# Kernel optimization log

Measured on AMD Instinct MI355X. Metric: run time of the kernel, lower is better.

The kernel has to match this reference:

```python
import jax, jax.numpy as jnp
import numpy as np
import math

B, S, N, D, H = 4, 64, 256, 512, 8
DEPTH = D // H

def setup_inputs() -> dict:
    key = jax.random.key(0)
    ks = jax.random.split(key, 9)
    scale = 1.0 / math.sqrt(D)
    return {
        "x": jax.random.normal(ks[0], (B, S, N, D), dtype=jnp.float32),
        "Wq": jax.random.normal(ks[1], (D, D), dtype=jnp.float32) * scale,
        "bq": jax.random.normal(ks[2], (D,), dtype=jnp.float32) * 0.01,
        "Wk": jax.random.normal(ks[3], (D, D), dtype=jnp.float32) * scale,
        "bk": jax.random.normal(ks[4], (D,), dtype=jnp.float32) * 0.01,
        "Wv": jax.random.normal(ks[5], (D, D), dtype=jnp.float32) * scale,
        "bv": jax.random.normal(ks[6], (D,), dtype=jnp.float32) * 0.01,
        "Wo": jax.random.normal(ks[7], (D, D), dtype=jnp.float32) * scale,
        "bo": jax.random.normal(ks[8], (D,), dtype=jnp.float32) * 0.01,
    }

def _split_heads(t):
    # (B, S, M, D) -> (B, H, S, M, depth); matches split_head.forward (4D path)
    # followed by the att_dim==2 permute(0, 2, 1, 3, 4) in cross_attention.
    b, s, m, _ = t.shape
    return t.reshape(b, s, m, H, DEPTH).transpose(0, 3, 1, 2, 4)

def reference(x, Wq, bq, Wk, bk, Wv, bv, Wo, bo):
    b, s, n, d = x.shape
    # att_dim == 2: query is the cls token along the joint/patch axis.
    q = _split_heads(x[:, :, 0:1, :] @ Wq + bq)   # (B, H, S, 1, depth)
    k = _split_heads(x @ Wk + bk)                  # (B, H, S, N, depth)
    v = _split_heads(x @ Wv + bv)                  # (B, H, S, N, depth)
    # scaled dot product attention (mask is None in cross_attention)
    logits = jnp.einsum('bhsqd,bhskd->bhsqk', q, k) / math.sqrt(DEPTH)
    attn = jax.nn.softmax(logits, axis=-1)         # (B, H, S, 1, N)
    ctx = jnp.einsum('bhsqk,bhskd->bhsqd', attn, v)  # (B, H, S, 1, depth)
    # permute(0, 2, 3, 1, 4) then reshape (B, S, 1, D)
    concat = ctx.transpose(0, 2, 3, 1, 4).reshape(b, s, 1, d)
    return concat @ Wo + bo
```

## Files before the change

### kernel.cpp

```cpp
#include <hip/hip_runtime.h>
#include <stdint.h>
#include <math.h>


#define NT 32

__global__ __launch_bounds__(512) void fused_kernel(
    const float* __restrict__ x,
    const float* __restrict__ Wq, const float* __restrict__ bq,
    const float* __restrict__ Wk,
    const float* __restrict__ Wv, const float* __restrict__ bv,
    const float* __restrict__ Wo, const float* __restrict__ bo,
    float* __restrict__ out) {
  const int bs = blockIdx.x;
  const int t = threadIdx.x;
  const int w = t >> 6, lane = t & 63;
  const float* xb = x + (long)bs * 131072;

  __shared__ float x_tile[NT * 512];
  __shared__ float r_s[4096];
  __shared__ float y_s[8 * 520];
  __shared__ float q_s[512];
  __shared__ float x0_s[512];
  __shared__ float ctx_s[512];
  __shared__ float red_s[3][512];
  __shared__ float pt_s[8][NT];
  __shared__ float f_s[8], s_s[8];

  if (t < 128) *(float4*)&x0_s[t * 4] = *(const float4*)&xb[t * 4];
  __syncthreads();

  {
    const int j4 = (t & 127) * 4;
    const int kq = t >> 7;
    float4 a = make_float4(0.f, 0.f, 0.f, 0.f);
    const float* wp = Wq + (long)(kq * 128) * 512 + j4;
    const float* ap = &x0_s[kq * 128];
#pragma unroll 8
    for (int k = 0; k < 128; ++k) {
      float4 wv = *(const float4*)&wp[(long)k * 512];
      float av = ap[k];
      a.x += av * wv.x; a.y += av * wv.y; a.z += av * wv.z; a.w += av * wv.w;
    }
    if (kq > 0) *(float4*)&red_s[kq - 1][j4] = a;
    __syncthreads();
    if (kq == 0) {
#pragma unroll
      for (int rr = 0; rr < 3; ++rr) {
        float4 b = *(const float4*)&red_s[rr][j4];
        a.x += b.x; a.y += b.y; a.z += b.z; a.w += b.w;
      }
      float4 bb = *(const float4*)&bq[j4];
      a.x += bb.x; a.y += bb.y; a.z += bb.z; a.w += bb.w;
      *(float4*)&q_s[j4] = a;
    }
  }
  __syncthreads();

  {
    const float* wrow = Wk + (long)t * 512;
    for (int h = 0; h < 8; ++h) {
      float racc = 0.f;
      const float* qp = &q_s[h * 64];
#pragma unroll
      for (int c4 = 0; c4 < 16; ++c4) {
        float4 wv = *(const float4*)&wrow[h * 64 + c4 * 4];
        racc += qp[c4 * 4 + 0] * wv.x + qp[c4 * 4 + 1] * wv.y +
                qp[c4 * 4 + 2] * wv.z + qp[c4 * 4 + 3] * wv.w;
      }
      r_s[h * 512 + t] = racc;
    }
  }
  __syncthreads();

  float rv[8][8];
#pragma unroll
  for (int h = 0; h < 8; ++h) {
    float4 a = *(const float4*)&r_s[h * 512 + lane * 8];
    float4 b = *(const float4*)&r_s[h * 512 + lane * 8 + 4];
    rv[h][0] = a.x; rv[h][1] = a.y; rv[h][2] = a.z; rv[h][3] = a.w;
    rv[h][4] = b.x; rv[h][5] = b.y; rv[h][6] = b.z; rv[h][7] = b.w;
  }

  float accy[8] = {0.f, 0.f, 0.f, 0.f, 0.f, 0.f, 0.f, 0.f};
  float m_h = -INFINITY, s_h = 0.f;
  const int l4 = lane & 4, l2 = lane & 2, l1 = lane & 1;

  for (int tile = 0; tile < 8; ++tile) {
    {
      const float* src = xb + (long)tile * NT * 512;
#pragma unroll
      for (int i = 0; i < 8; ++i) {
        int f4 = t + i * 512;
        *(float4*)&x_tile[f4 * 4] = *(const float4*)&src[f4 * 4];
      }
    }
    __syncthreads();

#pragma unroll
    for (int i = 0; i < 4; ++i) {
      const int nl = w * 4 + i;
      const float* xr = &x_tile[nl * 512 + lane * 8];
      float4 xa = *(const float4*)xr;
      float4 xb4 = *(const float4*)(xr + 4);
      float acc[8];
#pragma unroll
      for (int h = 0; h < 8; ++h)
        acc[h] = xa.x * rv[h][0] + xa.y * rv[h][1] + xa.z * rv[h][2] + xa.w * rv[h][3]
               + xb4.x * rv[h][4] + xb4.y * rv[h][5] + xb4.z * rv[h][6] + xb4.w * rv[h][7];
#pragma unroll
      for (int j = 0; j < 4; ++j) {
        float v = l4 ? acc[j] : acc[j + 4];
        float tt = __shfl_xor(v, 4);
        acc[j] = (l4 ? acc[j + 4] : acc[j]) + tt;
      }
#pragma unroll
      for (int j = 0; j < 2; ++j) {
        float v = l2 ? acc[j] : acc[j + 2];
        float tt = __shfl_xor(v, 2);
        acc[j] = (l2 ? acc[j + 2] : acc[j]) + tt;
      }
      {
        float v = l1 ? acc[0] : acc[1];
        float tt = __shfl_xor(v, 1);
        acc[0] = (l1 ? acc[1] : acc[0]) + tt;
      }
      acc[0] += __shfl_xor(acc[0], 8);
      acc[0] += __shfl_xor(acc[0], 16);
      acc[0] += __shfl_xor(acc[0], 32);
      if (lane < 8) pt_s[lane][nl] = acc[0] * 0.125f;
    }
    __syncthreads();

    {
      float l = (lane < 32) ? pt_s[w][lane] : -INFINITY;
      float tm = l;
#pragma unroll
      for (int o = 16; o; o >>= 1) tm = fmaxf(tm, __shfl_xor(tm, o));
      float m_new = fmaxf(m_h, tm);
      float e = __expf(l - m_new);
      float ts = e;
#pragma unroll
      for (int o = 16; o; o >>= 1) ts += __shfl_xor(ts, o);
      float f = __expf(m_h - m_new);
      s_h = s_h * f + ts;
      m_h = m_new;
      if (lane == 0) f_s[w] = f;
      if (lane < 32) pt_s[w][lane] = e;
    }
    __syncthreads();

    {
#pragma unroll
      for (int h = 0; h < 8; ++h) accy[h] *= f_s[h];
#pragma unroll 4
      for (int n4 = 0; n4 < 8; ++n4) {
        float xv0 = x_tile[(n4 * 4 + 0) * 512 + t];
        float xv1 = x_tile[(n4 * 4 + 1) * 512 + t];
        float xv2 = x_tile[(n4 * 4 + 2) * 512 + t];
        float xv3 = x_tile[(n4 * 4 + 3) * 512 + t];
#pragma unroll
        for (int h = 0; h < 8; ++h) {
          float4 p4 = *(const float4*)&pt_s[h][n4 * 4];
          accy[h] += p4.x * xv0 + p4.y * xv1 + p4.z * xv2 + p4.w * xv3;
        }
      }
    }
    __syncthreads();
  }

  if (lane == 0) s_s[w] = s_h;
  __syncthreads();
#pragma unroll
  for (int h = 0; h < 8; ++h) y_s[h * 520 + t] = accy[h] * (1.f / s_s[h]);
  __syncthreads();

  {
    const int o4 = (t & 127) * 4;
    const int kq = t >> 7;
    const int h0 = o4 >> 6;
    float4 a = make_float4(0.f, 0.f, 0.f, 0.f);
    const float* wp = Wv + (long)(kq * 128) * 512 + o4;
    const float* yp = &y_s[h0 * 520 + kq * 128];
#pragma unroll 8
    for (int k = 0; k < 128; ++k) {
      float4 wv = *(const float4*)&wp[(long)k * 512];
      float yv = yp[k];
      a.x += yv * wv.x; a.y += yv * wv.y; a.z += yv * wv.z; a.w += yv * wv.w;
    }
    if (kq > 0) *(float4*)&red_s[kq - 1][o4] = a;
    __syncthreads();
    if (kq == 0) {
#pragma unroll
      for (int rr = 0; rr < 3; ++rr) {
        float4 b = *(const float4*)&red_s[rr][o4];
        a.x += b.x; a.y += b.y; a.z += b.z; a.w += b.w;
      }
      float4 bb = *(const float4*)&bv[o4];
      a.x += bb.x; a.y += bb.y; a.z += bb.z; a.w += bb.w;
      *(float4*)&ctx_s[o4] = a;
    }
  }
  __syncthreads();

  {
    const int j4 = (t & 127) * 4;
    const int kq = t >> 7;
    float4 a = make_float4(0.f, 0.f, 0.f, 0.f);
    const float* wp = Wo + (long)(kq * 128) * 512 + j4;
    const float* cp = &ctx_s[kq * 128];
#pragma unroll 8
    for (int k = 0; k < 128; ++k) {
      float4 wv = *(const float4*)&wp[(long)k * 512];
      float cv = cp[k];
      a.x += cv * wv.x; a.y += cv * wv.y; a.z += cv * wv.z; a.w += cv * wv.w;
    }
    if (kq > 0) *(float4*)&red_s[kq - 1][j4] = a;
    __syncthreads();
    if (kq == 0) {
#pragma unroll
      for (int rr = 0; rr < 3; ++rr) {
        float4 b = *(const float4*)&red_s[rr][j4];
        a.x += b.x; a.y += b.y; a.z += b.z; a.w += b.w;
      }
      float4 bb = *(const float4*)&bo[j4];
      a.x += bb.x; a.y += bb.y; a.z += bb.z; a.w += bb.w;
      *(float4*)&out[(long)bs * 512 + j4] = a;
    }
  }
}

extern "C" void kernel_launch(void* const* d_in, const int* in_sizes, int n_in,
                              void* d_out, int out_size, void* d_ws, size_t ws_size,
                              hipStream_t stream) {
  (void)in_sizes; (void)n_in; (void)out_size; (void)d_ws; (void)ws_size;
  const float* x  = (const float*)d_in[0];
  const float* Wq = (const float*)d_in[1];
  const float* bq = (const float*)d_in[2];
  const float* Wk = (const float*)d_in[3];
  const float* Wv = (const float*)d_in[5];
  const float* bv = (const float*)d_in[6];
  const float* Wo = (const float*)d_in[7];
  const float* bo = (const float*)d_in[8];
  float* out = (float*)d_out;

  fused_kernel<<<256, 512, 0, stream>>>(x, Wq, bq, Wk, Wv, bv, Wo, bo, out);
}
```

Before: 288.7 us.

## Double-buffer x tiles with register prefetch and double block size to 1024 threads

The block grows from 512 to 1024 threads. The x tile shrinks to 16 rows and is double-buffered in shared memory: the next tile is loaded into registers while the current one is processed, so global loads overlap compute and the first tile is fetched before the projection work. The score and value-accumulation phases are split across the larger thread count, with a final cross-half reduction of the y accumulators, and the small GEMVs use an 8-way K split. The cost is higher register pressure at 1024 threads, more shared memory, and twice as many tile iterations, each with its own barriers.

```diff
diff --git a/kernel.cpp b/kernel.cpp
--- a/kernel.cpp
+++ b/kernel.cpp
@@ -3,9 +3,9 @@
 #include <math.h>
 
 
-#define NT 32
-
-__global__ __launch_bounds__(512) void fused_kernel(
+#define NT 16
+
+__global__ __launch_bounds__(1024) void fused_kernel(
     const float* __restrict__ x,
     const float* __restrict__ Wq, const float* __restrict__ bq,
     const float* __restrict__ Wk,
@@ -17,27 +17,30 @@
   const int w = t >> 6, lane = t & 63;
   const float* xb = x + (long)bs * 131072;
 
-  __shared__ float x_tile[NT * 512];
+  __shared__ float xt[2][NT * 512];
   __shared__ float r_s[4096];
   __shared__ float y_s[8 * 520];
+  __shared__ float ypar[8][512];
+  __shared__ float red_s[7][512];
   __shared__ float q_s[512];
   __shared__ float x0_s[512];
   __shared__ float ctx_s[512];
-  __shared__ float red_s[3][512];
   __shared__ float pt_s[8][NT];
   __shared__ float f_s[8], s_s[8];
 
   if (t < 128) *(float4*)&x0_s[t * 4] = *(const float4*)&xb[t * 4];
+  float4 st0 = *(const float4*)&xb[(long)t * 4];
+  float4 st1 = *(const float4*)&xb[(long)(t + 1024) * 4];
   __syncthreads();
 
   {
     const int j4 = (t & 127) * 4;
     const int kq = t >> 7;
     float4 a = make_float4(0.f, 0.f, 0.f, 0.f);
-    const float* wp = Wq + (long)(kq * 128) * 512 + j4;
-    const float* ap = &x0_s[kq * 128];
+    const float* wp = Wq + (long)(kq * 64) * 512 + j4;
+    const float* ap = &x0_s[kq * 64];
 #pragma unroll 8
-    for (int k = 0; k < 128; ++k) {
+    for (int k = 0; k < 64; ++k) {
       float4 wv = *(const float4*)&wp[(long)k * 512];
       float av = ap[k];
       a.x += av * wv.x; a.y += av * wv.y; a.z += av * wv.z; a.w += av * wv.w;
@@ -46,7 +49,7 @@
     __syncthreads();
     if (kq == 0) {
 #pragma unroll
-      for (int rr = 0; rr < 3; ++rr) {
+      for (int rr = 0; rr < 7; ++rr) {
         float4 b = *(const float4*)&red_s[rr][j4];
         a.x += b.x; a.y += b.y; a.z += b.z; a.w += b.w;
       }
@@ -58,19 +61,24 @@
   __syncthreads();
 
   {
-    const float* wrow = Wk + (long)t * 512;
-    for (int h = 0; h < 8; ++h) {
+    const int d = t >> 1, hh = t & 1;
+    const float* wrow = Wk + (long)d * 512 + hh * 256;
+#pragma unroll
+    for (int hi = 0; hi < 4; ++hi) {
+      const int h = hh * 4 + hi;
+      const float* qp = &q_s[h * 64];
       float racc = 0.f;
-      const float* qp = &q_s[h * 64];
 #pragma unroll
       for (int c4 = 0; c4 < 16; ++c4) {
-        float4 wv = *(const float4*)&wrow[h * 64 + c4 * 4];
+        float4 wv = *(const float4*)&wrow[hi * 64 + c4 * 4];
         racc += qp[c4 * 4 + 0] * wv.x + qp[c4 * 4 + 1] * wv.y +
                 qp[c4 * 4 + 2] * wv.z + qp[c4 * 4 + 3] * wv.w;
       }
-      r_s[h * 512 + t] = racc;
-    }
-  }
+      r_s[h * 512 + d] = racc;
+    }
+  }
+  *(float4*)&xt[0][t * 4] = st0;
+  *(float4*)&xt[0][(t + 1024) * 4] = st1;
   __syncthreads();
 
   float rv[8][8];
@@ -85,22 +93,19 @@
   float accy[8] = {0.f, 0.f, 0.f, 0.f, 0.f, 0.f, 0.f, 0.f};
   float m_h = -INFINITY, s_h = 0.f;
   const int l4 = lane & 4, l2 = lane & 2, l1 = lane & 1;
-
-  for (int tile = 0; tile < 8; ++tile) {
+  const int dcol = t & 511, halfn = t >> 9;
+
+  for (int tile = 0; tile < 16; ++tile) {
+    const int cur = tile & 1;
+    float4 n0, n1;
+    if (tile < 15) {
+      const float* src = xb + (long)(tile + 1) * NT * 512;
+      n0 = *(const float4*)&src[(long)t * 4];
+      n1 = *(const float4*)&src[(long)(t + 1024) * 4];
+    }
+
     {
-      const float* src = xb + (long)tile * NT * 512;
-#pragma unroll
-      for (int i = 0; i < 8; ++i) {
-        int f4 = t + i * 512;
-        *(float4*)&x_tile[f4 * 4] = *(const float4*)&src[f4 * 4];
-      }
-    }
-    __syncthreads();
-
-#pragma unroll
-    for (int i = 0; i < 4; ++i) {
-      const int nl = w * 4 + i;
-      const float* xr = &x_tile[nl * 512 + lane * 8];
+      const float* xr = &xt[cur][w * 512 + lane * 8];
       float4 xa = *(const float4*)xr;
       float4 xb4 = *(const float4*)(xr + 4);
       float acc[8];
@@ -128,40 +133,46 @@
       acc[0] += __shfl_xor(acc[0], 8);
       acc[0] += __shfl_xor(acc[0], 16);
       acc[0] += __shfl_xor(acc[0], 32);
-      if (lane < 8) pt_s[lane][nl] = acc[0] * 0.125f;
-    }
-    __syncthreads();
-
-    {
-      float l = (lane < 32) ? pt_s[w][lane] : -INFINITY;
+      if (lane < 8) pt_s[lane][w] = acc[0] * 0.125f;
+    }
+    __syncthreads();
+
+    if (w < 8) {
+      float l = (lane < 16) ? pt_s[w][lane] : -3.0e38f;
       float tm = l;
 #pragma unroll
-      for (int o = 16; o; o >>= 1) tm = fmaxf(tm, __shfl_xor(tm, o));
+      for (int o = 8; o; o >>= 1) tm = fmaxf(tm, __shfl_xor(tm, o));
       float m_new = fmaxf(m_h, tm);
       float e = __expf(l - m_new);
       float ts = e;
 #pragma unroll
-      for (int o = 16; o; o >>= 1) ts += __shfl_xor(ts, o);
+      for (int o = 8; o; o >>= 1) ts += __shfl_xor(ts, o);
       float f = __expf(m_h - m_new);
       s_h = s_h * f + ts;
       m_h = m_new;
       if (lane == 0) f_s[w] = f;
-      if (lane < 32) pt_s[w][lane] = e;
-    }
-    __syncthreads();
+      if (lane < 16) pt_s[w][lane] = e;
+    }
+    __syncthreads();
+
+    if (tile < 15) {
+      *(float4*)&xt[cur ^ 1][t * 4] = n0;
+      *(float4*)&xt[cur ^ 1][(t + 1024) * 4] = n1;
+    }
 
     {
 #pragma unroll
       for (int h = 0; h < 8; ++h) accy[h] *= f_s[h];
-#pragma unroll 4
-      for (int n4 = 0; n4 < 8; ++n4) {
-        float xv0 = x_tile[(n4 * 4 + 0) * 512 + t];
-        float xv1 = x_tile[(n4 * 4 + 1) * 512 + t];
-        float xv2 = x_tile[(n4 * 4 + 2) * 512 + t];
-        float xv3 = x_tile[(n4 * 4 + 3) * 512 + t];
+#pragma unroll
+      for (int n4 = 0; n4 < 2; ++n4) {
+        const int nb = halfn * 8 + n4 * 4;
+        float xv0 = xt[cur][(nb + 0) * 512 + dcol];
+        float xv1 = xt[cur][(nb + 1) * 512 + dcol];
+        float xv2 = xt[cur][(nb + 2) * 512 + dcol];
+        float xv3 = xt[cur][(nb + 3) * 512 + dcol];
 #pragma unroll
         for (int h = 0; h < 8; ++h) {
-          float4 p4 = *(const float4*)&pt_s[h][n4 * 4];
+          float4 p4 = *(const float4*)&pt_s[h][nb];
           accy[h] += p4.x * xv0 + p4.y * xv1 + p4.z * xv2 + p4.w * xv3;
         }
       }
@@ -169,10 +180,18 @@
     __syncthreads();
   }
 
-  if (lane == 0) s_s[w] = s_h;
-  __syncthreads();
-#pragma unroll
-  for (int h = 0; h < 8; ++h) y_s[h * 520 + t] = accy[h] * (1.f / s_s[h]);
+  if (w < 8 && lane == 0) s_s[w] = s_h;
+  __syncthreads();
+  if (halfn == 1) {
+#pragma unroll
+    for (int h = 0; h < 8; ++h) ypar[h][dcol] = accy[h];
+  }
+  __syncthreads();
+  if (halfn == 0) {
+#pragma unroll
+    for (int h = 0; h < 8; ++h)
+      y_s[h * 520 + dcol] = (accy[h] + ypar[h][dcol]) * (1.f / s_s[h]);
+  }
   __syncthreads();
 
   {
@@ -180,19 +199,19 @@
     const int kq = t >> 7;
     const int h0 = o4 >> 6;
     float4 a = make_float4(0.f, 0.f, 0.f, 0.f);
-    const float* wp = Wv + (long)(kq * 128) * 512 + o4;
-    const float* yp = &y_s[h0 * 520 + kq * 128];
+    const float* wp = Wv + (long)(kq * 64) * 512 + o4;
+    const float* yp2 = &y_s[h0 * 520 + kq * 64];
 #pragma unroll 8
-    for (int k = 0; k < 128; ++k) {
+    for (int k = 0; k < 64; ++k) {
       float4 wv = *(const float4*)&wp[(long)k * 512];
-      float yv = yp[k];
+      float yv = yp2[k];
       a.x += yv * wv.x; a.y += yv * wv.y; a.z += yv * wv.z; a.w += yv * wv.w;
     }
     if (kq > 0) *(float4*)&red_s[kq - 1][o4] = a;
     __syncthreads();
     if (kq == 0) {
 #pragma unroll
-      for (int rr = 0; rr < 3; ++rr) {
+      for (int rr = 0; rr < 7; ++rr) {
         float4 b = *(const float4*)&red_s[rr][o4];
         a.x += b.x; a.y += b.y; a.z += b.z; a.w += b.w;
       }
@@ -207,10 +226,10 @@
     const int j4 = (t & 127) * 4;
     const int kq = t >> 7;
     float4 a = make_float4(0.f, 0.f, 0.f, 0.f);
-    const float* wp = Wo + (long)(kq * 128) * 512 + j4;
-    const float* cp = &ctx_s[kq * 128];
+    const float* wp = Wo + (long)(kq * 64) * 512 + j4;
+    const float* cp = &ctx_s[kq * 64];
 #pragma unroll 8
-    for (int k = 0; k < 128; ++k) {
+    for (int k = 0; k < 64; ++k) {
       float4 wv = *(const float4*)&wp[(long)k * 512];
       float cv = cp[k];
       a.x += cv * wv.x; a.y += cv * wv.y; a.z += cv * wv.z; a.w += cv * wv.w;
@@ -219,7 +238,7 @@
     __syncthreads();
     if (kq == 0) {
 #pragma unroll
-      for (int rr = 0; rr < 3; ++rr) {
+      for (int rr = 0; rr < 7; ++rr) {
         float4 b = *(const float4*)&red_s[rr][j4];
         a.x += b.x; a.y += b.y; a.z += b.z; a.w += b.w;
       }
@@ -244,5 +263,5 @@
   const float* bo = (const float*)d_in[8];
   float* out = (float*)d_out;
 
-  fused_kernel<<<256, 512, 0, stream>>>(x, Wq, bq, Wk, Wv, bv, Wo, bo, out);
+  fused_kernel<<<256, 1024, 0, stream>>>(x, Wq, bq, Wk, Wv, bv, Wo, bo, out);
 }
```

After: 283.4 us. Within noise of the previous version (-1.9%).
